# Optimization experiments

Measured on AMD Instinct MI355X. Metric: run time of the kernel, lower is better.

The kernel has to match this reference:

```python
import jax, jax.numpy as jnp
import numpy as np

B, S, HID = 2, 2048, 2048
H, KVH, D = 16, 4, 128
GROUPS = H // KVH  # 4


def apply_rotary(x, cos, sin):
    # x: [B, h, S, D]; cos/sin: [S, D//2]
    xr = x[..., 0::2]
    xi = x[..., 1::2]
    c = cos[None, None, :, :]
    s = sin[None, None, :, :]
    orr = xr * c - xi * s
    oi = xr * s + xi * c
    return jnp.stack([orr, oi], axis=-1).reshape(x.shape)


def setup_inputs() -> dict:
    key = jax.random.key(0)
    k0, k1, k2, k3, k4 = jax.random.split(key, 5)
    x = jax.random.normal(k0, (B, S, HID), dtype=jnp.float32)
    # real RoPE frequencies (llama-style), stored as [S, D//2, 2] = (cos, sin)
    inv_freq = 1.0 / (10000.0 ** (np.arange(0, D, 2, dtype=np.float32) / D))
    t = np.arange(S, dtype=np.float32)
    ang = np.outer(t, inv_freq)  # [S, D//2]
    freqs_cis = jnp.asarray(np.stack([np.cos(ang), np.sin(ang)], axis=-1), dtype=jnp.float32)
    sc = 0.02
    wq = jax.random.normal(k1, (HID, H * D), dtype=jnp.float32) * sc
    wk = jax.random.normal(k2, (HID, KVH * D), dtype=jnp.float32) * sc
    wv = jax.random.normal(k3, (HID, KVH * D), dtype=jnp.float32) * sc
    wo = jax.random.normal(k4, (H * D, HID), dtype=jnp.float32) * sc
    return {"x": x, "freqs_cis": freqs_cis, "wq": wq, "wk": wk, "wv": wv, "wo": wo}


def reference(x, freqs_cis, wq, wk, wv, wo):
    b, s, _ = x.shape
    cos, sin = freqs_cis[..., 0], freqs_cis[..., 1]
    q = (x @ wq).reshape(b, s, H, D).transpose(0, 2, 1, 3)    # [B,H,S,D]
    k = (x @ wk).reshape(b, s, KVH, D).transpose(0, 2, 1, 3)  # [B,KVH,S,D]
    v = (x @ wv).reshape(b, s, KVH, D).transpose(0, 2, 1, 3)
    q = apply_rotary(q, cos, sin)
    k = apply_rotary(k, cos, sin)
    # GQA expand: repeat kv heads into query-head groups
    k = jnp.repeat(k, GROUPS, axis=1)  # [B,H,S,D]
    v = jnp.repeat(v, GROUPS, axis=1)
    scale = 1.0 / jnp.sqrt(jnp.asarray(D, dtype=x.dtype))
    scores = jnp.einsum("bhqd,bhkd->bhqk", q, k) * scale
    causal = jnp.tril(jnp.ones((s, s), dtype=bool))
    scores = jnp.where(causal[None, None], scores, jnp.asarray(-jnp.inf, dtype=scores.dtype))
    attn = jax.nn.softmax(scores, axis=-1)
    out = jnp.einsum("bhqk,bhkd->bhqd", attn, v)
    out = out.transpose(0, 2, 1, 3).reshape(b, s, H * D)
    return out @ wo
```

## Files before the change

kernel.cpp:

```cpp
#include <hip/hip_runtime.h>
#include <hip/hip_bf16.h>

#define B_   2
#define S_   2048
#define HID_ 2048
#define H_   16
#define KVH_ 4
#define D_   128
#define M_   4096
#define NQKV 3072

typedef __attribute__((ext_vector_type(8))) short bf16x8;
typedef __attribute__((ext_vector_type(4))) float f32x4;
typedef const __attribute__((address_space(1))) unsigned int* gas_p;
typedef __attribute__((address_space(3))) unsigned int* las_p;

__device__ __forceinline__ unsigned short f2b(float f) {
    __hip_bfloat16 h = __float2bfloat16(f);
    return *reinterpret_cast<unsigned short*>(&h);
}
__device__ __forceinline__ float b2f(unsigned short u) {
    __hip_bfloat16 h;
    *reinterpret_cast<unsigned short*>(&h) = u;
    return __bfloat162float(h);
}

__global__ __launch_bounds__(256)
void convert_x(const float* __restrict__ x, unsigned short* __restrict__ xb) {
    int i = (blockIdx.x * 256 + threadIdx.x) * 4;
    float4 v = *(const float4*)(x + i);
    ushort4 o;
    o.x = f2b(v.x); o.y = f2b(v.y); o.z = f2b(v.z); o.w = f2b(v.w);
    *(ushort4*)(xb + i) = o;
}

__global__ __launch_bounds__(256)
void convert_w_all(const float* __restrict__ wq, const float* __restrict__ wk,
                   const float* __restrict__ wv, const float* __restrict__ wo,
                   unsigned short* __restrict__ wqkvT,
                   unsigned short* __restrict__ woT) {
    __shared__ float tile[32][33];
    int z = blockIdx.z;
    const float* w; int N, nbase; unsigned short* dst;
    if (z == 0)      { w = wq; N = 2048; nbase = 0;    dst = wqkvT; }
    else if (z == 1) { w = wk; N = 512;  nbase = 2048; dst = wqkvT; }
    else if (z == 2) { w = wv; N = 512;  nbase = 2560; dst = wqkvT; }
    else             { w = wo; N = 2048; nbase = 0;    dst = woT; }
    int n0 = blockIdx.x * 32, k0 = blockIdx.y * 32;
    if (n0 >= N) return;
    int tx = threadIdx.x & 31, ty = threadIdx.x >> 5;
    #pragma unroll
    for (int j = 0; j < 4; j++)
        tile[ty + j*8][tx] = w[(size_t)(k0 + ty + j*8) * N + n0 + tx];
    __syncthreads();
    #pragma unroll
    for (int j = 0; j < 4; j++)
        dst[(size_t)(nbase + n0 + ty + j*8) * 2048 + k0 + tx] = f2b(tile[tx][ty + j*8]);
}

#define BAR    asm volatile("s_barrier" ::: "memory")
#define GATE2  asm volatile("s_waitcnt vmcnt(2)" ::: "memory")
#define GATE4  asm volatile("s_waitcnt vmcnt(4)" ::: "memory")
#define GATE6  asm volatile("s_waitcnt vmcnt(6)" ::: "memory")
#define GATE8  asm volatile("s_waitcnt vmcnt(8)" ::: "memory")
#define PHI    __builtin_amdgcn_s_setprio(1)
#define PLO    __builtin_amdgcn_s_setprio(0)

#define STG(srcrow, ldsbase, half, tile) do {                                   \
    _Pragma("unroll")                                                           \
    for (int it_ = 0; it_ < 2; ++it_) {                                         \
      int p_ = w * 128 + it_ * 64 + lane;                                       \
      int r_ = (half) * 128 + (p_ >> 3);                                        \
      int q8_ = ((p_ & 7) ^ ((p_ >> 3) & 7)) * 8;                               \
      __builtin_amdgcn_global_load_lds(                                         \
          (gas_p)((srcrow) + (size_t)r_ * 2048 + (tile) * 64 + q8_),            \
          (las_p)((char*)(ldsbase) + ((half) * 1024 + w * 128 + it_ * 64) * 16),\
          16, 0, 0);                                                            \
    } } while (0)

#define RDA2(dst, bufi, mi) do {                                                \
    const unsigned short* Ab_ = &As[bufi][0] + (mi)*8192 + wr*4096 + l15*64;    \
    _Pragma("unroll")                                                           \
    for (int f_ = 0; f_ < 4; ++f_) {                                            \
      dst[f_][0] = *(const bf16x8*)(Ab_ + f_*1024 + slot0);                     \
      dst[f_][1] = *(const bf16x8*)(Ab_ + f_*1024 + slot1);                     \
    } } while (0)

#define RDB2(dst, bufi, ni) do {                                                \
    const unsigned short* Bb_ = &Bs[bufi][0] + (ni)*8192 + wc*2048 + l15*64;    \
    _Pragma("unroll")                                                           \
    for (int g_ = 0; g_ < 2; ++g_) {                                            \
      dst[g_][0] = *(const bf16x8*)(Bb_ + g_*1024 + slot0);                     \
      dst[g_][1] = *(const bf16x8*)(Bb_ + g_*1024 + slot1);                     \
    } } while (0)

#define MMQ(ra, rb, mi, ni) do {                                                \
    _Pragma("unroll")                                                           \
    for (int f_ = 0; f_ < 4; ++f_)                                              \
      _Pragma("unroll")                                                         \
      for (int g_ = 0; g_ < 2; ++g_) {                                          \
        acc[(mi)*4+f_][(ni)*2+g_] = __builtin_amdgcn_mfma_f32_16x16x32_bf16(    \
            ra[f_][0], rb[g_][0], acc[(mi)*4+f_][(ni)*2+g_], 0, 0, 0);          \
        acc[(mi)*4+f_][(ni)*2+g_] = __builtin_amdgcn_mfma_f32_16x16x32_bf16(    \
            ra[f_][1], rb[g_][1], acc[(mi)*4+f_][(ni)*2+g_], 0, 0, 0);          \
      } } while (0)

__global__ __launch_bounds__(512)
void gemm8(const unsigned short* __restrict__ A,
           const unsigned short* __restrict__ BT,
           unsigned short* __restrict__ qkvb,
           unsigned short* __restrict__ vTb,
           const float* __restrict__ freqs) {
    __shared__ unsigned short As[2][16384];
    __shared__ unsigned short Bs[2][16384];

    int tid  = threadIdx.x;
    int lane = tid & 63, w = tid >> 6;
    int l15  = lane & 15, quad = lane >> 4;
    int wr = w >> 2, wc = w & 3;
    int bid = blockIdx.y * 12 + blockIdx.x;
    int s_  = (bid & 7) * 24 + (bid >> 3);
    int by  = s_ / 12, bx = s_ % 12;
    int row0 = by * 256, col0 = bx * 256;
    int slot0 = (quad ^ (lane & 7)) * 8;
    int slot1 = slot0 ^ 32;

    const unsigned short* Arow = A  + (size_t)row0 * 2048;
    const unsigned short* Brow = BT + (size_t)col0 * 2048;

    f32x4 acc[8][4];
    #pragma unroll
    for (int i = 0; i < 8; ++i)
        #pragma unroll
        for (int j = 0; j < 4; ++j) acc[i][j] = f32x4{0.f, 0.f, 0.f, 0.f};

    bf16x8 ra0[4][2], ra1[4][2];
    bf16x8 rb0[2][2], rb1[2][2];

    STG(Brow, &Bs[0][0], 0, 0);
    STG(Arow, &As[0][0], 0, 0);
    STG(Arow, &As[0][0], 1, 0);
    STG(Brow, &Bs[0][0], 1, 0);
    STG(Brow, &Bs[1][0], 0, 1);
    STG(Arow, &As[1][0], 0, 1);
    STG(Arow, &As[1][0], 1, 1);
    STG(Brow, &Bs[1][0], 1, 1);
    GATE8;
    BAR;
    RDB2(rb0, 0, 0);
    RDA2(ra0, 0, 0);

    #pragma unroll 1
    for (int i = 0; i < 16; ++i) {
        int t  = 2 * i;
        int t2 = (t + 2 > 31) ? 31 : t + 2;
        int t3 = (t + 3 > 31) ? 31 : t + 3;
        RDA2(ra1, 0, 1);
        PHI; MMQ(ra0, rb0, 0, 0); PLO;
        STG(Brow, &Bs[0][0], 0, t2);
        BAR;
        RDB2(rb1, 0, 1);
        PHI; MMQ(ra1, rb0, 1, 0); PLO;
        STG(Arow, &As[0][0], 0, t2);
        GATE8; BAR;
        RDB2(rb0, 1, 0);
        PHI; MMQ(ra0, rb1, 0, 1); PLO;
        STG(Arow, &As[0][0], 1, t2);
        BAR;
        RDA2(ra0, 1, 0);
        PHI; MMQ(ra1, rb1, 1, 1); PLO;
        STG(Brow, &Bs[0][0], 1, t2);
        GATE8; BAR;
        RDA2(ra1, 1, 1);
        PHI; MMQ(ra0, rb0, 0, 0); PLO;
        STG(Brow, &Bs[1][0], 0, t3);
        BAR;
        RDB2(rb1, 1, 1);
        PHI; MMQ(ra1, rb0, 1, 0); PLO;
        STG(Arow, &As[1][0], 0, t3);
        GATE8; BAR;
        RDB2(rb0, 0, 0);
        PHI; MMQ(ra0, rb1, 0, 1); PLO;
        STG(Arow, &As[1][0], 1, t3);
        BAR;
        RDA2(ra0, 0, 0);
        PHI; MMQ(ra1, rb1, 1, 1); PLO;
        STG(Brow, &Bs[1][0], 1, t3);
        GATE8; BAR;
    }

    int q4 = quad * 4;
    if (col0 < 2560) {
        #pragma unroll
        for (int mi = 0; mi < 2; ++mi)
        #pragma unroll
        for (int f = 0; f < 4; ++f) {
            int mb = row0 + mi*128 + wr*64 + f*16 + q4;
            #pragma unroll
            for (int ni = 0; ni < 2; ++ni)
            #pragma unroll
            for (int g = 0; g < 2; ++g) {
                int colb = col0 + ni*128 + wc*32 + g*16 + l15;
                int dd = (colb & 127) & ~1;
                bool odd = colb & 1;
                #pragma unroll
                for (int rr = 0; rr < 4; ++rr) {
                    int m = mb + rr;
                    int s = m & 2047;
                    float v  = acc[mi*4 + f][ni*2 + g][rr];
                    float pv = __shfl_xor(v, 1);
                    float cs = freqs[s*128 + dd];
                    float sn = freqs[s*128 + dd + 1];
                    float o  = odd ? (pv*sn + v*cs) : (v*cs - pv*sn);
                    qkvb[(size_t)m * NQKV + colb] = f2b(o);
                }
            }
        }
    } else {
        #pragma unroll
        for (int mi = 0; mi < 2; ++mi)
        #pragma unroll
        for (int f = 0; f < 4; ++f) {
            int mb = row0 + mi*128 + wr*64 + f*16 + q4;
            int s0 = mb & 2047;
            #pragma unroll
            for (int ni = 0; ni < 2; ++ni)
            #pragma unroll
            for (int g = 0; g < 2; ++g) {
                int colb = col0 + ni*128 + wc*32 + g*16 + l15;
                int vrow = (row0 >> 11) * 512 + (colb - 2560);
                ushort4 ov;
                ov.x = f2b(acc[mi*4 + f][ni*2 + g][0]);
                ov.y = f2b(acc[mi*4 + f][ni*2 + g][1]);
                ov.z = f2b(acc[mi*4 + f][ni*2 + g][2]);
                ov.w = f2b(acc[mi*4 + f][ni*2 + g][3]);
                *(ushort4*)(vTb + (size_t)vrow * 2048 + s0) = ov;
            }
        }
    }
}

#define STGO(srcrow, ldsbase, unit, tile) do {                                  \
    _Pragma("unroll")                                                           \
    for (int it_ = 0; it_ < 2; ++it_) {                                         \
      int p_ = w * 128 + it_ * 64 + lane;                                       \
      int r_ = (unit) * 64 + (p_ >> 3);                                         \
      int q8_ = ((p_ & 7) ^ ((p_ >> 3) & 7)) * 8;                               \
      __builtin_amdgcn_global_load_lds(                                         \
          (gas_p)((srcrow) + (size_t)r_ * 2048 + (tile) * 64 + q8_),            \
          (las_p)((char*)(ldsbase) + ((unit) * 512 + w * 128 + it_ * 64) * 16), \
          16, 0, 0);                                                            \
    } } while (0)

#define RDA3(dst, bufi, pp) do {                                                \
    const unsigned short* Ab_ = &As[bufi][0] + wr*4096 + l15*64;                \
    _Pragma("unroll")                                                           \
    for (int f_ = 0; f_ < 2; ++f_) {                                            \
      dst[f_][0] = *(const bf16x8*)(Ab_ + ((pp)*2+f_)*1024 + slot0);            \
      dst[f_][1] = *(const bf16x8*)(Ab_ + ((pp)*2+f_)*1024 + slot1);            \
    } } while (0)

#define RDB3(dst, bufi, pp) do {                                                \
    const unsigned short* Bb_ = &Bs[bufi][0] + wc*4096 + l15*64;                \
    _Pragma("unroll")                                                           \
    for (int g_ = 0; g_ < 2; ++g_) {                                            \
      dst[g_][0] = *(const bf16x8*)(Bb_ + ((pp)*2+g_)*1024 + slot0);            \
      dst[g_][1] = *(const bf16x8*)(Bb_ + ((pp)*2+g_)*1024 + slot1);            \
    } } while (0)

#define MMQ3(ra, rb, mi, ni) do {                                               \
    _Pragma("unroll")                                                           \
    for (int f_ = 0; f_ < 2; ++f_)                                              \
      _Pragma("unroll")                                                         \
      for (int g_ = 0; g_ < 2; ++g_) {                                          \
        acc[(mi)*2+f_][(ni)*2+g_] = __builtin_amdgcn_mfma_f32_16x16x32_bf16(    \
            ra[f_][0], rb[g_][0], acc[(mi)*2+f_][(ni)*2+g_], 0, 0, 0);          \
        acc[(mi)*2+f_][(ni)*2+g_] = __builtin_amdgcn_mfma_f32_16x16x32_bf16(    \
            ra[f_][1], rb[g_][1], acc[(mi)*2+f_][(ni)*2+g_], 0, 0, 0);          \
      } } while (0)

__global__ __launch_bounds__(256)
void gemm8o(const unsigned short* __restrict__ A,
            const unsigned short* __restrict__ BT,
            float* __restrict__ Cf) {
    __shared__ unsigned short As[2][8192];
    __shared__ unsigned short Bs[2][8192];

    int tid  = threadIdx.x;
    int lane = tid & 63, w = tid >> 6;
    int l15  = lane & 15, quad = lane >> 4;
    int wr = w >> 1, wc = w & 1;
    int bid = blockIdx.y * 16 + blockIdx.x;
    int s_  = (bid & 7) * 64 + (bid >> 3);
    int by  = s_ >> 4, bx = s_ & 15;
    int row0 = by * 128, col0 = bx * 128;
    int slot0 = (quad ^ (lane & 7)) * 8;
    int slot1 = slot0 ^ 32;

    const unsigned short* Arow = A  + (size_t)row0 * 2048;
    const unsigned short* Brow = BT + (size_t)col0 * 2048;

    f32x4 acc[4][4];
    #pragma unroll
    for (int i = 0; i < 4; ++i)
        #pragma unroll
        for (int j = 0; j < 4; ++j) acc[i][j] = f32x4{0.f, 0.f, 0.f, 0.f};

    bf16x8 a0[2][2], a1[2][2], b0[2][2], b1[2][2];

    STGO(Arow, &As[0][0], 0, 0);
    STGO(Arow, &As[0][0], 1, 0);
    STGO(Brow, &Bs[0][0], 0, 0);
    STGO(Brow, &Bs[0][0], 1, 0);
    STGO(Arow, &As[1][0], 0, 1);
    STGO(Brow, &Bs[1][0], 0, 1);
    STGO(Brow, &Bs[1][0], 1, 1);
    GATE6;
    BAR;
    RDB3(b0, 0, 0);
    RDA3(a0, 0, 0);

    #pragma unroll 1
    for (int i = 0; i < 16; ++i) {
        int t  = 2 * i;
        int t2 = (t + 2 > 31) ? 31 : t + 2;
        int t3 = (t + 3 > 31) ? 31 : t + 3;
        RDA3(a1, 0, 1);
        PHI; MMQ3(a0, b0, 0, 0); PLO;
        STGO(Arow, &As[1][0], 1, t + 1);
        BAR;
        RDB3(b1, 0, 1);
        PHI; MMQ3(a1, b0, 1, 0); PLO;
        STGO(Arow, &As[0][0], 0, t2);
        GATE2; BAR;
        RDB3(b0, 1, 0);
        PHI; MMQ3(a0, b1, 0, 1); PLO;
        STGO(Arow, &As[0][0], 1, t2);
        BAR;
        RDA3(a0, 1, 0);
        PHI; MMQ3(a1, b1, 1, 1); PLO;
        STGO(Brow, &Bs[0][0], 0, t2);
        GATE4; BAR;
        RDA3(a1, 1, 1);
        PHI; MMQ3(a0, b0, 0, 0); PLO;
        STGO(Brow, &Bs[0][0], 1, t2);
        BAR;
        RDB3(b1, 1, 1);
        PHI; MMQ3(a1, b0, 1, 0); PLO;
        STGO(Arow, &As[1][0], 0, t3);
        GATE2; BAR;
        RDB3(b0, 0, 0);
        PHI; MMQ3(a0, b1, 0, 1); PLO;
        STGO(Brow, &Bs[1][0], 0, t3);
        BAR;
        RDA3(a0, 0, 0);
        PHI; MMQ3(a1, b1, 1, 1); PLO;
        STGO(Brow, &Bs[1][0], 1, t3);
        GATE4; BAR;
    }

    int q4 = quad * 4;
    #pragma unroll
    for (int f = 0; f < 4; ++f) {
        int mb = row0 + wr*64 + f*16 + q4;
        #pragma unroll
        for (int g = 0; g < 4; ++g) {
            int colb = col0 + wc*64 + g*16 + l15;
            #pragma unroll
            for (int rr = 0; rr < 4; ++rr)
                Cf[(size_t)(mb + rr) * 2048 + colb] = acc[f][g][rr];
        }
    }
}

__global__ __launch_bounds__(512)
void attn_mfma(const unsigned short* __restrict__ qkv,
               const unsigned short* __restrict__ vT,
               unsigned short* __restrict__ ao,
               unsigned short* __restrict__ wsP,
               float2* __restrict__ wsML) {
    __shared__ unsigned short Ks[64 * 128];
    __shared__ unsigned short Vt[128 * 64];

    int tid  = threadIdx.x;
    int lane = tid & 63, w = tid >> 6;
    int quad = lane >> 4, l15 = lane & 15;
    int hw = w >> 1, qhalf = w & 1;
    int bx = blockIdx.x, hk = blockIdx.y, b = blockIdx.z;
    int h = hk * 4 + hw;

    int qt, c;
    if (bx < 12)      { qt = 31 - bx / 3;        c = bx % 3; }
    else if (bx < 40) { qt = 27 - (bx - 12) / 2; c = (bx - 12) & 1; }
    else              { qt = 53 - bx;            c = 0; }
    int nt = qt + 1;
    int nch = (qt >= 28) ? 3 : (qt >= 14 ? 2 : 1);
    int kt_begin = c * 14;
    int kt_end = (nt < (c + 1) * 14) ? nt : (c + 1) * 14;
    bool lastc = (c == nch - 1);
    int q0 = qt * 64;
    const float scale = 0.08838834764831845f;

    bf16x8 aq[2][4];
    #pragma unroll
    for (int qf = 0; qf < 2; qf++) {
        const unsigned short* qrow =
            qkv + (size_t)(b*2048 + q0 + qhalf*32 + qf*16 + l15) * NQKV + h*128;
        #pragma unroll
        for (int k4 = 0; k4 < 4; k4++)
            aq[qf][k4] = *(const bf16x8*)(qrow + k4*32 + quad*8);
    }

    int koff[4][4];
    #pragma unroll
    for (int j = 0; j < 4; j++) {
        int row = ((j >> 1) * 32) + ((l15 >> 2) * 8) + ((j & 1) * 4) + (l15 & 3);
        #pragma unroll
        for (int k4 = 0; k4 < 4; k4++) {
            int slot = (k4 * 4 + quad) ^ (row & 15);
            koff[j][k4] = (row * 16 + slot) * 8;
        }
    }
    int vbase0 = (l15 * 8 + (quad ^ (l15 & 7))) * 8;
    int vbase1 = (l15 * 8 + ((4 + quad) ^ (l15 & 7))) * 8;

    const unsigned short* kb0 = qkv + (size_t)(b*2048) * NQKV + 2048 + hk*128;
    const unsigned short* vb0 = vT + (size_t)(b*512 + hk*128) * 2048;

    auto stage_k = [&](int kt) {
        #pragma unroll
        for (int it = 0; it < 2; it++) {
            int s = w * 128 + it * 64 + lane;
            int r = s >> 4, qp = s & 15;
            int q = qp ^ (r & 15);
            __builtin_amdgcn_global_load_lds(
                (gas_p)(kb0 + (size_t)(kt*64 + r) * NQKV + q * 8),
                (las_p)((char*)&Ks[0] + (w * 128 + it * 64) * 16),
                16, 0, 0);
        }
    };
    auto stage_v = [&](int kt) {
        #pragma unroll
        for (int it = 0; it < 2; it++) {
            int s = w * 128 + it * 64 + lane;
            int r = s >> 3, qp = s & 7;
            int q = qp ^ (r & 7);
            __builtin_amdgcn_global_load_lds(
                (gas_p)(vb0 + (size_t)r * 2048 + kt*64 + q * 8),
                (las_p)((char*)&Vt[0] + (w * 128 + it * 64) * 16),
                16, 0, 0);
        }
    };

    f32x4 o_acc[2][8];
    const f32x4 zf = {0.f, 0.f, 0.f, 0.f};
    #pragma unroll
    for (int qf = 0; qf < 2; qf++)
        #pragma unroll
        for (int jn = 0; jn < 8; jn++) o_acc[qf][jn] = zf;
    float m_i[2] = {-1e30f, -1e30f}, l_i[2] = {0.f, 0.f};
    int qglob[2] = {q0 + qhalf*32 + l15, q0 + qhalf*32 + 16 + l15};

    stage_k(kt_begin);
    for (int kt = kt_begin; kt < kt_end; kt++) {
        __syncthreads();
        stage_v(kt);

        f32x4 s_acc[2][4];
        #pragma unroll
        for (int j = 0; j < 4; j++) {
            s_acc[0][j] = zf; s_acc[1][j] = zf;
            #pragma unroll
            for (int k4 = 0; k4 < 4; k4++) {
                bf16x8 ak = *(const bf16x8*)&Ks[koff[j][k4]];
                s_acc[0][j] = __builtin_amdgcn_mfma_f32_16x16x32_bf16(ak, aq[0][k4], s_acc[0][j], 0, 0, 0);
                s_acc[1][j] = __builtin_amdgcn_mfma_f32_16x16x32_bf16(ak, aq[1][k4], s_acc[1][j], 0, 0, 0);
            }
        }

        bf16x8 pp[2][2];
        #pragma unroll
        for (int qf = 0; qf < 2; qf++) {
            float sv[4][4];
            #pragma unroll
            for (int j = 0; j < 4; j++)
                #pragma unroll
                for (int r = 0; r < 4; r++)
                    sv[j][r] = s_acc[qf][j][r] * scale;
            if (kt == qt) {
                #pragma unroll
                for (int j = 0; j < 4; j++)
                    #pragma unroll
                    for (int r = 0; r < 4; r++) {
                        int sloc = ((j >> 1) * 32) + quad*8 + ((j & 1) * 4) + r;
                        if (kt*64 + sloc > qglob[qf]) sv[j][r] = -1e30f;
                    }
            }
            float mx = sv[0][0];
            #pragma unroll
            for (int j = 0; j < 4; j++)
                #pragma unroll
                for (int r = 0; r < 4; r++) mx = fmaxf(mx, sv[j][r]);
            mx = fmaxf(mx, __shfl_xor(mx, 16));
            mx = fmaxf(mx, __shfl_xor(mx, 32));
            float mnew = fmaxf(m_i[qf], mx);
            float alpha = __expf(m_i[qf] - mnew);
            float rs = 0.f;
            float p[4][4];
            #pragma unroll
            for (int j = 0; j < 4; j++)
                #pragma unroll
                for (int r = 0; r < 4; r++) {
                    p[j][r] = __expf(sv[j][r] - mnew);
                    rs += p[j][r];
                }
            l_i[qf] = l_i[qf] * alpha + rs;
            m_i[qf] = mnew;
            #pragma unroll
            for (int jn = 0; jn < 8; jn++)
                #pragma unroll
                for (int r = 0; r < 4; r++) o_acc[qf][jn][r] *= alpha;
            #pragma unroll
            for (int r = 0; r < 4; r++) {
                pp[qf][0][r]     = (short)f2b(p[0][r]);
                pp[qf][0][r + 4] = (short)f2b(p[1][r]);
                pp[qf][1][r]     = (short)f2b(p[2][r]);
                pp[qf][1][r + 4] = (short)f2b(p[3][r]);
            }
        }

        __syncthreads();
        if (kt + 1 < kt_end) stage_k(kt + 1);

        #pragma unroll
        for (int jn = 0; jn < 8; jn++) {
            bf16x8 av0 = *(const bf16x8*)&Vt[jn*1024 + vbase0];
            bf16x8 av1 = *(const bf16x8*)&Vt[jn*1024 + vbase1];
            o_acc[0][jn] = __builtin_amdgcn_mfma_f32_16x16x32_bf16(av0, pp[0][0], o_acc[0][jn], 0, 0, 0);
            o_acc[0][jn] = __builtin_amdgcn_mfma_f32_16x16x32_bf16(av1, pp[0][1], o_acc[0][jn], 0, 0, 0);
            o_acc[1][jn] = __builtin_amdgcn_mfma_f32_16x16x32_bf16(av0, pp[1][0], o_acc[1][jn], 0, 0, 0);
            o_acc[1][jn] = __builtin_amdgcn_mfma_f32_16x16x32_bf16(av1, pp[1][1], o_acc[1][jn], 0, 0, 0);
        }
    }

    int pi = 0, mi = 0;
    if (qt >= 14) {
        if (qt < 28) { mi = (qt - 14) * 2 + c;       pi = qt - 14; }
        else         { mi = 28 + (qt - 28) * 3 + c;  pi = 14 + (qt - 28) * 2 + c; }
    }
    #pragma unroll
    for (int qf = 0; qf < 2; qf++) {
        float lt = l_i[qf];
        lt += __shfl_xor(lt, 16);
        lt += __shfl_xor(lt, 32);
        float inv = 1.f / lt;
        int q_local = qhalf * 32 + qf * 16 + l15;
        unsigned short* dst;
        if (lastc)
            dst = ao + (size_t)(b*2048 + q0 + q_local) * 2048 + h*128;
        else
            dst = wsP + (size_t)(((pi * 8 + hk * 2 + b) * 4 + hw) * 64 + q_local) * 128;
        #pragma unroll
        for (int jn = 0; jn < 8; jn++) {
            ushort4 ov;
            ov.x = f2b(o_acc[qf][jn][0] * inv);
            ov.y = f2b(o_acc[qf][jn][1] * inv);
            ov.z = f2b(o_acc[qf][jn][2] * inv);
            ov.w = f2b(o_acc[qf][jn][3] * inv);
            *(ushort4*)(dst + jn*16 + quad*4) = ov;
        }
        if (qt >= 14 && quad == 0)
            wsML[(mi * 8 + hk * 2 + b) * 256 + hw * 64 + q_local]
                = make_float2(m_i[qf], lt);
    }
}

__global__ __launch_bounds__(256)
void merge_kernel(unsigned short* __restrict__ ao,
                  const unsigned short* __restrict__ wsP,
                  const float2* __restrict__ wsML) {
    int t = blockIdx.x * 256 + threadIdx.x;
    int d = (t & 15) * 8;
    int h = (t >> 4) & 15;
    int rest = t >> 8;
    int q_off = rest % 1152;
    int b = rest / 1152;
    int q = 896 + q_off;
    int qt = q >> 6, q_local = q & 63;
    int hk = h >> 2, hw = h & 3;
    int nch = (qt >= 28) ? 3 : 2;

    float mv[3], lv[3];
    for (int cc = 0; cc < nch; cc++) {
        int mi = (qt < 28) ? (qt - 14) * 2 + cc : 28 + (qt - 28) * 3 + cc;
        float2 ml = wsML[(mi * 8 + hk * 2 + b) * 256 + hw * 64 + q_local];
        mv[cc] = ml.x; lv[cc] = ml.y;
    }
    float M = mv[0];
    for (int cc = 1; cc < nch; cc++) M = fmaxf(M, mv[cc]);
    float f[3], S = 0.f;
    for (int cc = 0; cc < nch; cc++) { f[cc] = __expf(mv[cc] - M) * lv[cc]; S += f[cc]; }
    float inv = 1.f / S;

    unsigned short* arow = ao + (size_t)(b*2048 + q) * 2048 + h*128 + d;
    float outv[8];
    {
        ushort4 a0 = *(ushort4*)arow, a1 = *(ushort4*)(arow + 4);
        float fl = f[nch-1];
        outv[0] = fl*b2f(a0.x); outv[1] = fl*b2f(a0.y);
        outv[2] = fl*b2f(a0.z); outv[3] = fl*b2f(a0.w);
        outv[4] = fl*b2f(a1.x); outv[5] = fl*b2f(a1.y);
        outv[6] = fl*b2f(a1.z); outv[7] = fl*b2f(a1.w);
    }
    for (int cc = 0; cc < nch - 1; cc++) {
        int pi = (qt < 28) ? (qt - 14) : 14 + (qt - 28) * 2 + cc;
        const unsigned short* prow =
            wsP + (size_t)(((pi * 8 + hk * 2 + b) * 4 + hw) * 64 + q_local) * 128 + d;
        ushort4 p0 = *(const ushort4*)prow, p1 = *(const ushort4*)(prow + 4);
        float fc = f[cc];
        outv[0] += fc*b2f(p0.x); outv[1] += fc*b2f(p0.y);
        outv[2] += fc*b2f(p0.z); outv[3] += fc*b2f(p0.w);
        outv[4] += fc*b2f(p1.x); outv[5] += fc*b2f(p1.y);
        outv[6] += fc*b2f(p1.z); outv[7] += fc*b2f(p1.w);
    }
    ushort4 o0, o1;
    o0.x = f2b(outv[0]*inv); o0.y = f2b(outv[1]*inv);
    o0.z = f2b(outv[2]*inv); o0.w = f2b(outv[3]*inv);
    o1.x = f2b(outv[4]*inv); o1.y = f2b(outv[5]*inv);
    o1.z = f2b(outv[6]*inv); o1.w = f2b(outv[7]*inv);
    *(ushort4*)arow = o0;
    *(ushort4*)(arow + 4) = o1;
}

extern "C" void kernel_launch(void* const* d_in, const int* in_sizes, int n_in,
                              void* d_out, int out_size, void* d_ws, size_t ws_size,
                              hipStream_t stream) {
    const float* x     = (const float*)d_in[0];
    const float* freqs = (const float*)d_in[1];
    const float* wq    = (const float*)d_in[2];
    const float* wk    = (const float*)d_in[3];
    const float* wv    = (const float*)d_in[4];
    const float* wo    = (const float*)d_in[5];
    float* out = (float*)d_out;

    char* ws = (char*)d_ws;
    unsigned short* xbf    = (unsigned short*)(ws);
    unsigned short* aobuf  = (unsigned short*)(ws);
    unsigned short* wqkvT  = (unsigned short*)(ws + (16u<<20));
    unsigned short* woT    = (unsigned short*)(ws + (28u<<20));
    unsigned short* qkvbuf = (unsigned short*)(ws + (36u<<20));
    unsigned short* vTbuf  = (unsigned short*)(ws + (60u<<20));
    unsigned short* wsP  = (unsigned short*)(ws + (16u<<20));
    float2*         wsML = (float2*)(ws + (16u<<20) + 176u*65536u);

    dim3 blk(256);
    convert_x<<<8192, blk, 0, stream>>>(x, xbf);
    convert_w_all<<<dim3(64, 64, 4), blk, 0, stream>>>(wq, wk, wv, wo, wqkvT, woT);
    gemm8<<<dim3(NQKV/256, M_/256), dim3(512), 0, stream>>>(
        xbf, wqkvT, qkvbuf, vTbuf, freqs);
    attn_mfma<<<dim3(54, 4, 2), dim3(512), 0, stream>>>(qkvbuf, vTbuf, aobuf, wsP, wsML);
    merge_kernel<<<2304, blk, 0, stream>>>(aobuf, wsP, wsML);
    gemm8o<<<dim3(2048/128, M_/128), blk, 0, stream>>>(aobuf, woT, out);
}
```

Measured before the change: 328.7 us.

## Retile output GEMM, fold softmax scale into Q, defer rescale in attention

Several changes land together. The QKV GEMM loop now issues its global-to-LDS stages before each MFMA block rather than after it. The attention scale is folded into Q in the QKV epilogue, and the online softmax skips the alpha rescale of O and l when a wavefront's new max stays within 8 of the running max, removing exp and multiply work per tile. The output GEMM moves to 256x128 tiles with 512 threads, a new barrier/lgkmcnt-gated schedule and a peeled tail, aiming for better reuse and MFMA density. The extra barriers and lgkmcnt waits could add stalls, and the deferred max lets exponentials reach up to e^8 before rescaling.

```diff
diff --git a/kernel.cpp b/kernel.cpp
--- a/kernel.cpp
+++ b/kernel.cpp
@@ -59,8 +59,9 @@
 }
 
 #define BAR    asm volatile("s_barrier" ::: "memory")
-#define GATE2  asm volatile("s_waitcnt vmcnt(2)" ::: "memory")
-#define GATE4  asm volatile("s_waitcnt vmcnt(4)" ::: "memory")
+#define LG0    do { asm volatile("s_waitcnt lgkmcnt(0)" ::: "memory"); \
+                    __builtin_amdgcn_sched_barrier(0); } while (0)
+#define GATE0  asm volatile("s_waitcnt vmcnt(0)" ::: "memory")
 #define GATE6  asm volatile("s_waitcnt vmcnt(6)" ::: "memory")
 #define GATE8  asm volatile("s_waitcnt vmcnt(8)" ::: "memory")
 #define PHI    __builtin_amdgcn_s_setprio(1)
@@ -156,41 +157,42 @@
         int t2 = (t + 2 > 31) ? 31 : t + 2;
         int t3 = (t + 3 > 31) ? 31 : t + 3;
         RDA2(ra1, 0, 1);
+        STG(Brow, &Bs[0][0], 0, t2);
         PHI; MMQ(ra0, rb0, 0, 0); PLO;
-        STG(Brow, &Bs[0][0], 0, t2);
         BAR;
         RDB2(rb1, 0, 1);
+        STG(Arow, &As[0][0], 0, t2);
         PHI; MMQ(ra1, rb0, 1, 0); PLO;
-        STG(Arow, &As[0][0], 0, t2);
         GATE8; BAR;
         RDB2(rb0, 1, 0);
+        STG(Arow, &As[0][0], 1, t2);
         PHI; MMQ(ra0, rb1, 0, 1); PLO;
-        STG(Arow, &As[0][0], 1, t2);
         BAR;
         RDA2(ra0, 1, 0);
+        STG(Brow, &Bs[0][0], 1, t2);
         PHI; MMQ(ra1, rb1, 1, 1); PLO;
-        STG(Brow, &Bs[0][0], 1, t2);
         GATE8; BAR;
         RDA2(ra1, 1, 1);
+        STG(Brow, &Bs[1][0], 0, t3);
         PHI; MMQ(ra0, rb0, 0, 0); PLO;
-        STG(Brow, &Bs[1][0], 0, t3);
         BAR;
         RDB2(rb1, 1, 1);
+        STG(Arow, &As[1][0], 0, t3);
         PHI; MMQ(ra1, rb0, 1, 0); PLO;
-        STG(Arow, &As[1][0], 0, t3);
         GATE8; BAR;
         RDB2(rb0, 0, 0);
+        STG(Arow, &As[1][0], 1, t3);
         PHI; MMQ(ra0, rb1, 0, 1); PLO;
-        STG(Arow, &As[1][0], 1, t3);
         BAR;
         RDA2(ra0, 0, 0);
+        STG(Brow, &Bs[1][0], 1, t3);
         PHI; MMQ(ra1, rb1, 1, 1); PLO;
-        STG(Brow, &Bs[1][0], 1, t3);
         GATE8; BAR;
     }
 
     int q4 = quad * 4;
     if (col0 < 2560) {
+        const float qscale = 0.08838834764831845f;
         #pragma unroll
         for (int mi = 0; mi < 2; ++mi)
         #pragma unroll
@@ -203,6 +205,7 @@
                 int colb = col0 + ni*128 + wc*32 + g*16 + l15;
                 int dd = (colb & 127) & ~1;
                 bool odd = colb & 1;
+                float sc = (colb < 2048) ? qscale : 1.f;
                 #pragma unroll
                 for (int rr = 0; rr < 4; ++rr) {
                     int m = mb + rr;
@@ -212,7 +215,7 @@
                     float cs = freqs[s*128 + dd];
                     float sn = freqs[s*128 + dd + 1];
                     float o  = odd ? (pv*sn + v*cs) : (v*cs - pv*sn);
-                    qkvb[(size_t)m * NQKV + colb] = f2b(o);
+                    qkvb[(size_t)m * NQKV + colb] = f2b(o * sc);
                 }
             }
         }
@@ -240,50 +243,36 @@
     }
 }
 
-#define STGO(srcrow, ldsbase, unit, tile) do {                                  \
+#define RDAo(bufi) do {                                                         \
+    const unsigned short* Ab_ = &As[bufi][0] + wr * 4096 + l15 * 64;            \
     _Pragma("unroll")                                                           \
-    for (int it_ = 0; it_ < 2; ++it_) {                                         \
-      int p_ = w * 128 + it_ * 64 + lane;                                       \
-      int r_ = (unit) * 64 + (p_ >> 3);                                         \
-      int q8_ = ((p_ & 7) ^ ((p_ >> 3) & 7)) * 8;                               \
-      __builtin_amdgcn_global_load_lds(                                         \
-          (gas_p)((srcrow) + (size_t)r_ * 2048 + (tile) * 64 + q8_),            \
-          (las_p)((char*)(ldsbase) + ((unit) * 512 + w * 128 + it_ * 64) * 16), \
-          16, 0, 0);                                                            \
+    for (int f_ = 0; f_ < 4; ++f_) {                                            \
+      af[f_][0] = *(const bf16x8*)(Ab_ + f_ * 1024 + slot0);                    \
+      af[f_][1] = *(const bf16x8*)(Ab_ + f_ * 1024 + slot1);                    \
     } } while (0)
 
-#define RDA3(dst, bufi, pp) do {                                                \
-    const unsigned short* Ab_ = &As[bufi][0] + wr*4096 + l15*64;                \
+#define RDBo(bufi, g) do {                                                      \
+    const unsigned short* Bb_ = &Bs[bufi][0] + wc * 4096 + l15 * 64;            \
+    bfr[g][0] = *(const bf16x8*)(Bb_ + (g) * 1024 + slot0);                     \
+    bfr[g][1] = *(const bf16x8*)(Bb_ + (g) * 1024 + slot1);                     \
+    } while (0)
+
+#define MM8o(mi, ni) do {                                                       \
     _Pragma("unroll")                                                           \
-    for (int f_ = 0; f_ < 2; ++f_) {                                            \
-      dst[f_][0] = *(const bf16x8*)(Ab_ + ((pp)*2+f_)*1024 + slot0);            \
-      dst[f_][1] = *(const bf16x8*)(Ab_ + ((pp)*2+f_)*1024 + slot1);            \
-    } } while (0)
-
-#define RDB3(dst, bufi, pp) do {                                                \
-    const unsigned short* Bb_ = &Bs[bufi][0] + wc*4096 + l15*64;                \
-    _Pragma("unroll")                                                           \
-    for (int g_ = 0; g_ < 2; ++g_) {                                            \
-      dst[g_][0] = *(const bf16x8*)(Bb_ + ((pp)*2+g_)*1024 + slot0);            \
-      dst[g_][1] = *(const bf16x8*)(Bb_ + ((pp)*2+g_)*1024 + slot1);            \
-    } } while (0)
-
-#define MMQ3(ra, rb, mi, ni) do {                                               \
-    _Pragma("unroll")                                                           \
-    for (int f_ = 0; f_ < 2; ++f_)                                              \
+    for (int f_ = 2*(mi); f_ < 2*(mi)+2; ++f_)                                  \
       _Pragma("unroll")                                                         \
-      for (int g_ = 0; g_ < 2; ++g_) {                                          \
-        acc[(mi)*2+f_][(ni)*2+g_] = __builtin_amdgcn_mfma_f32_16x16x32_bf16(    \
-            ra[f_][0], rb[g_][0], acc[(mi)*2+f_][(ni)*2+g_], 0, 0, 0);          \
-        acc[(mi)*2+f_][(ni)*2+g_] = __builtin_amdgcn_mfma_f32_16x16x32_bf16(    \
-            ra[f_][1], rb[g_][1], acc[(mi)*2+f_][(ni)*2+g_], 0, 0, 0);          \
+      for (int g_ = 2*(ni); g_ < 2*(ni)+2; ++g_) {                              \
+        acc[f_][g_] = __builtin_amdgcn_mfma_f32_16x16x32_bf16(                  \
+            af[f_][0], bfr[g_][0], acc[f_][g_], 0, 0, 0);                       \
+        acc[f_][g_] = __builtin_amdgcn_mfma_f32_16x16x32_bf16(                  \
+            af[f_][1], bfr[g_][1], acc[f_][g_], 0, 0, 0);                       \
       } } while (0)
 
-__global__ __launch_bounds__(256)
+__global__ __launch_bounds__(512)
 void gemm8o(const unsigned short* __restrict__ A,
             const unsigned short* __restrict__ BT,
             float* __restrict__ Cf) {
-    __shared__ unsigned short As[2][8192];
+    __shared__ unsigned short As[2][16384];
     __shared__ unsigned short Bs[2][8192];
 
     int tid  = threadIdx.x;
@@ -291,9 +280,9 @@
     int l15  = lane & 15, quad = lane >> 4;
     int wr = w >> 1, wc = w & 1;
     int bid = blockIdx.y * 16 + blockIdx.x;
-    int s_  = (bid & 7) * 64 + (bid >> 3);
+    int s_  = (bid & 7) * 32 + (bid >> 3);
     int by  = s_ >> 4, bx = s_ & 15;
-    int row0 = by * 128, col0 = bx * 128;
+    int row0 = by * 256, col0 = bx * 128;
     int slot0 = (quad ^ (lane & 7)) * 8;
     int slot1 = slot0 ^ 32;
 
@@ -306,58 +295,50 @@
         #pragma unroll
         for (int j = 0; j < 4; ++j) acc[i][j] = f32x4{0.f, 0.f, 0.f, 0.f};
 
-    bf16x8 a0[2][2], a1[2][2], b0[2][2], b1[2][2];
-
-    STGO(Arow, &As[0][0], 0, 0);
-    STGO(Arow, &As[0][0], 1, 0);
-    STGO(Brow, &Bs[0][0], 0, 0);
-    STGO(Brow, &Bs[0][0], 1, 0);
-    STGO(Arow, &As[1][0], 0, 1);
-    STGO(Brow, &Bs[1][0], 0, 1);
-    STGO(Brow, &Bs[1][0], 1, 1);
+    bf16x8 af[4][2];
+    bf16x8 bfr[4][2];
+
+    STG(Arow, &As[0][0], 0, 0);
+    STG(Arow, &As[0][0], 1, 0);
+    STG(Brow, &Bs[0][0], 0, 0);
+    STG(Arow, &As[1][0], 0, 1);
+    STG(Arow, &As[1][0], 1, 1);
+    STG(Brow, &Bs[1][0], 0, 1);
     GATE6;
     BAR;
-    RDB3(b0, 0, 0);
-    RDA3(a0, 0, 0);
 
     #pragma unroll 1
-    for (int i = 0; i < 16; ++i) {
-        int t  = 2 * i;
-        int t2 = (t + 2 > 31) ? 31 : t + 2;
-        int t3 = (t + 3 > 31) ? 31 : t + 3;
-        RDA3(a1, 0, 1);
-        PHI; MMQ3(a0, b0, 0, 0); PLO;
-        STGO(Arow, &As[1][0], 1, t + 1);
-        BAR;
-        RDB3(b1, 0, 1);
-        PHI; MMQ3(a1, b0, 1, 0); PLO;
-        STGO(Arow, &As[0][0], 0, t2);
-        GATE2; BAR;
-        RDB3(b0, 1, 0);
-        PHI; MMQ3(a0, b1, 0, 1); PLO;
-        STGO(Arow, &As[0][0], 1, t2);
-        BAR;
-        RDA3(a0, 1, 0);
-        PHI; MMQ3(a1, b1, 1, 1); PLO;
-        STGO(Brow, &Bs[0][0], 0, t2);
-        GATE4; BAR;
-        RDA3(a1, 1, 1);
-        PHI; MMQ3(a0, b0, 0, 0); PLO;
-        STGO(Brow, &Bs[0][0], 1, t2);
-        BAR;
-        RDB3(b1, 1, 1);
-        PHI; MMQ3(a1, b0, 1, 0); PLO;
-        STGO(Arow, &As[1][0], 0, t3);
-        GATE2; BAR;
-        RDB3(b0, 0, 0);
-        PHI; MMQ3(a0, b1, 0, 1); PLO;
-        STGO(Brow, &Bs[1][0], 0, t3);
-        BAR;
-        RDA3(a0, 0, 0);
-        PHI; MMQ3(a1, b1, 1, 1); PLO;
-        STGO(Brow, &Bs[1][0], 1, t3);
-        GATE4; BAR;
-    }
+    for (int i = 0; i < 15; ++i) {
+        int t = 2 * i;
+        RDAo(0); RDBo(0, 0); RDBo(0, 1);
+        BAR; LG0; PHI; MM8o(0, 0); PLO; BAR;
+        RDBo(0, 2); RDBo(0, 3); STG(Arow, &As[0][0], 0, t + 2);
+        BAR; LG0; PHI; MM8o(0, 1); PLO; BAR;
+        STG(Arow, &As[0][0], 1, t + 2);
+        BAR; LG0; PHI; MM8o(1, 0); PLO; BAR;
+        STG(Brow, &Bs[0][0], 0, t + 2);
+        BAR; LG0; PHI; MM8o(1, 1); PLO; GATE6; BAR;
+        RDAo(1); RDBo(1, 0); RDBo(1, 1);
+        BAR; LG0; PHI; MM8o(0, 0); PLO; BAR;
+        RDBo(1, 2); RDBo(1, 3); STG(Arow, &As[1][0], 0, t + 3);
+        BAR; LG0; PHI; MM8o(0, 1); PLO; BAR;
+        STG(Arow, &As[1][0], 1, t + 3);
+        BAR; LG0; PHI; MM8o(1, 0); PLO; BAR;
+        STG(Brow, &Bs[1][0], 0, t + 3);
+        BAR; LG0; PHI; MM8o(1, 1); PLO; GATE6; BAR;
+    }
+    RDAo(0); RDBo(0, 0); RDBo(0, 1);
+    BAR; LG0; PHI; MM8o(0, 0); PLO; BAR;
+    RDBo(0, 2); RDBo(0, 3);
+    BAR; LG0; PHI; MM8o(0, 1); PLO; BAR;
+    BAR; LG0; PHI; MM8o(1, 0); PLO; BAR;
+    BAR; LG0; PHI; MM8o(1, 1); PLO; GATE0; BAR;
+    RDAo(1); RDBo(1, 0); RDBo(1, 1);
+    BAR; LG0; PHI; MM8o(0, 0); PLO; BAR;
+    RDBo(1, 2); RDBo(1, 3);
+    BAR; LG0; PHI; MM8o(0, 1); PLO; BAR;
+    BAR; LG0; PHI; MM8o(1, 0); PLO; BAR;
+    LG0; PHI; MM8o(1, 1); PLO;
 
     int q4 = quad * 4;
     #pragma unroll
@@ -399,7 +380,6 @@
     int kt_end = (nt < (c + 1) * 14) ? nt : (c + 1) * 14;
     bool lastc = (c == nch - 1);
     int q0 = qt * 64;
-    const float scale = 0.08838834764831845f;
 
     bf16x8 aq[2][4];
     #pragma unroll
@@ -486,7 +466,7 @@
             for (int j = 0; j < 4; j++)
                 #pragma unroll
                 for (int r = 0; r < 4; r++)
-                    sv[j][r] = s_acc[qf][j][r] * scale;
+                    sv[j][r] = s_acc[qf][j][r];
             if (kt == qt) {
                 #pragma unroll
                 for (int j = 0; j < 4; j++)
@@ -503,8 +483,8 @@
                 for (int r = 0; r < 4; r++) mx = fmaxf(mx, sv[j][r]);
             mx = fmaxf(mx, __shfl_xor(mx, 16));
             mx = fmaxf(mx, __shfl_xor(mx, 32));
-            float mnew = fmaxf(m_i[qf], mx);
-            float alpha = __expf(m_i[qf] - mnew);
+            int defer = __all(mx <= m_i[qf] + 8.f);
+            float mnew = defer ? m_i[qf] : fmaxf(m_i[qf], mx);
             float rs = 0.f;
             float p[4][4];
             #pragma unroll
@@ -514,12 +494,16 @@
                     p[j][r] = __expf(sv[j][r] - mnew);
                     rs += p[j][r];
                 }
-            l_i[qf] = l_i[qf] * alpha + rs;
-            m_i[qf] = mnew;
-            #pragma unroll
-            for (int jn = 0; jn < 8; jn++)
+            if (!defer) {
+                float alpha = __expf(m_i[qf] - mnew);
+                l_i[qf] *= alpha;
                 #pragma unroll
-                for (int r = 0; r < 4; r++) o_acc[qf][jn][r] *= alpha;
+                for (int jn = 0; jn < 8; jn++)
+                    #pragma unroll
+                    for (int r = 0; r < 4; r++) o_acc[qf][jn][r] *= alpha;
+                m_i[qf] = mnew;
+            }
+            l_i[qf] += rs;
             #pragma unroll
             for (int r = 0; r < 4; r++) {
                 pp[qf][0][r]     = (short)f2b(p[0][r]);
@@ -660,5 +644,5 @@
         xbf, wqkvT, qkvbuf, vTbuf, freqs);
     attn_mfma<<<dim3(54, 4, 2), dim3(512), 0, stream>>>(qkvbuf, vTbuf, aobuf, wsP, wsML);
     merge_kernel<<<2304, blk, 0, stream>>>(aobuf, wsP, wsML);
-    gemm8o<<<dim3(2048/128, M_/128), blk, 0, stream>>>(aobuf, woT, out);
-}
+    gemm8o<<<dim3(2048/128, M_/256), dim3(512), 0, stream>>>(aobuf, woT, out);
+}
```

Measured after the change: 319.3 us. 2.8% less time.
